# Kernel optimization log

Hardware: AMD Instinct MI355X
Metric: run time of the kernel (lower is better)

The kernel has to match this reference:

```python
import jax, jax.numpy as jnp
import numpy as np

ALPHA = 1.0
LORA_DIM = 4
MULTIPLIER = 1.0


def setup_inputs() -> dict:
    key = jax.random.key(0)
    ks = jax.random.split(key, 6)
    B, S, IN, OUT = 4, 4096, 4096, 4096
    x = jax.random.normal(ks[0], (B, S, IN), dtype=jnp.float32)
    W0 = jax.random.normal(ks[1], (OUT, IN), dtype=jnp.float32) * 0.02
    b = jax.random.normal(ks[2], (OUT,), dtype=jnp.float32) * 0.02
    # factorization(4096) -> (64, 64) for both in and out dims
    lokr_w1 = jax.random.normal(ks[3], (64, 64), dtype=jnp.float32) * 0.1
    lokr_w2_a = jax.random.normal(ks[4], (64, LORA_DIM), dtype=jnp.float32) * 0.1
    lokr_w2_b = jax.random.normal(ks[5], (LORA_DIM, 64), dtype=jnp.float32) * 0.1
    return {"x": x, "W0": W0, "b": b, "lokr_w1": lokr_w1,
            "lokr_w2_a": lokr_w2_a, "lokr_w2_b": lokr_w2_b}


def reference(x, W0, b, lokr_w1, lokr_w2_a, lokr_w2_b):
    # Original (frozen) linear forward
    result = jnp.einsum('bsi,oi->bso', x, W0) + b
    # LoKr delta weight: kron(w1, w2_a @ w2_b) * (alpha / lora_dim) * multiplier
    w2 = lokr_w2_a @ lokr_w2_b                      # (out_k, in_n) = (64, 64)
    scale = ALPHA / LORA_DIM
    diff_weight = jnp.kron(lokr_w1, w2) * (scale * MULTIPLIER)  # (4096, 4096)
    delta = jnp.einsum('bsi,oi->bso', x, diff_weight)
    return result + delta
```

## Files before the change

### kernel.cpp

```cpp
#include <hip/hip_runtime.h>
#include <hip/hip_bf16.h>
#include <stdint.h>

#define M_DIM 16384
#define N_DIM 4096
#define K_DIM 4096
#define NT    (K_DIM / 64)

typedef float f32x4 __attribute__((ext_vector_type(4)));
typedef short bf16x8 __attribute__((ext_vector_type(8)));
typedef unsigned short u16;

__device__ __forceinline__ unsigned short f32_to_bf16(float f) {
    union { float f; uint32_t u; } v; v.f = f;
    uint32_t u = v.u;
    uint32_t r = (u + 0x7FFFu + ((u >> 16) & 1u)) >> 16;
    return (unsigned short)r;
}

__device__ __forceinline__ void gload16(const void* g, void* l) {
    __builtin_amdgcn_global_load_lds(
        (const __attribute__((address_space(1))) void*)g,
        (__attribute__((address_space(3))) void*)l,
        16, 0, 0);
}

__global__ void build_weff(const float* __restrict__ W0,
                           const float* __restrict__ w1,
                           const float* __restrict__ w2a,
                           const float* __restrict__ w2b,
                           u16* __restrict__ Weff) {
    long idx = (long)blockIdx.x * 256 + threadIdx.x;
    long e0 = idx * 4;
    int o  = (int)(e0 >> 12);
    int i0 = (int)(e0 & 4095);
    int r  = o & 63;
    float a0 = w2a[r * 4 + 0], a1 = w2a[r * 4 + 1];
    float a2 = w2a[r * 4 + 2], a3 = w2a[r * 4 + 3];
    float w1v = w1[(o >> 6) * 64 + (i0 >> 6)] * 0.25f;
    float4 w0 = *(const float4*)(W0 + e0);
    const float* w0p = (const float*)&w0;
    unsigned short outp[4];
#pragma unroll
    for (int j = 0; j < 4; ++j) {
        int c = (i0 + j) & 63;
        float w2 = a0 * w2b[0 * 64 + c] + a1 * w2b[1 * 64 + c]
                 + a2 * w2b[2 * 64 + c] + a3 * w2b[3 * 64 + c];
        outp[j] = f32_to_bf16(w0p[j] + w1v * w2);
    }
    *(ushort4*)(Weff + e0) = make_ushort4(outp[0], outp[1], outp[2], outp[3]);
}

__global__ void cvt_x(const float* __restrict__ x, u16* __restrict__ xb) {
    long idx = (long)blockIdx.x * 256 + threadIdx.x;
    long e0 = idx * 8;
    float4 v0 = *(const float4*)(x + e0);
    float4 v1 = *(const float4*)(x + e0 + 4);
    union { unsigned short s[8]; int4 v; } o;
    const float* p0 = (const float*)&v0;
    const float* p1 = (const float*)&v1;
#pragma unroll
    for (int j = 0; j < 4; ++j) o.s[j]     = f32_to_bf16(p0[j]);
#pragma unroll
    for (int j = 0; j < 4; ++j) o.s[4 + j] = f32_to_bf16(p1[j]);
    *(int4*)(xb + e0) = o.v;
}

__global__ __launch_bounds__(512, 2) void gemm_8p(
        const u16* __restrict__ A,
        const u16* __restrict__ Bm,
        const float* __restrict__ bias,
        float* __restrict__ C) {
    __shared__ __align__(16) u16 ldsA[2][2][8192];
    __shared__ __align__(16) u16 ldsB[2][2][8192];

    const int tid = threadIdx.x;
    const int bid = blockIdx.x;
    const int swz = (bid & 7) * 128 + (bid >> 3);
    const int tm = swz >> 4;
    const int tn = swz & 15;
    const int mBase = tm * 256;
    const int nBase = tn * 256;

    const int lane = tid & 63;
    const int wave = tid >> 6;
    const int wr = wave >> 2;
    const int wc = wave & 3;

    const int srow = tid >> 2;
    const int slog = (tid & 3) ^ ((srow >> 1) & 3);
    const u16* aS0 = A  + (size_t)(mBase + srow)       * K_DIM + slog * 8;
    const u16* aS1 = A  + (size_t)(mBase + srow + 128) * K_DIM + slog * 8;
    const u16* bS0 = Bm + (size_t)(nBase + srow)       * K_DIM + slog * 8;
    const u16* bS1 = Bm + (size_t)(nBase + srow + 128) * K_DIM + slog * 8;

#define STAGE_A(buf, t, ks) do { const size_t _k = (size_t)(t) * 64 + (ks) * 32; \
        gload16(aS0 + _k, &ldsA[buf][ks][tid * 8]);                              \
        gload16(aS1 + _k, &ldsA[buf][ks][4096 + tid * 8]); } while (0)
#define STAGE_B(buf, t, ks) do { const size_t _k = (size_t)(t) * 64 + (ks) * 32; \
        gload16(bS0 + _k, &ldsB[buf][ks][tid * 8]);                              \
        gload16(bS1 + _k, &ldsB[buf][ks][4096 + tid * 8]); } while (0)

    const int rl = lane & 15, cbk = lane >> 4;
    const int sslot = cbk ^ ((rl >> 1) & 3);
    const int aRd = (wr * 128 + rl) * 32 + sslot * 8;
    const int bRd = (wc * 64  + rl) * 32 + sslot * 8;

#define RD_A(buf, ks, m) (*(const bf16x8*)&ldsA[buf][ks][aRd + (m) * 512])
#define RD_B(buf, ks, n) (*(const bf16x8*)&ldsB[buf][ks][bRd + (n) * 512])

    f32x4 acc[8][4] = {};
    bf16x8 aA0, aA1, aA2, aA3;
    bf16x8 aB0, aB1, aB2, aB3;
    bf16x8 bX0, bX1, bX2, bX3;
    bf16x8 bY0, bY1, bY2, bY3;

#define MFMA16(A0_,A1_,A2_,A3_,B0_,B1_,B2_,B3_,mh)                                      \
    acc[(mh)*4+0][0] = __builtin_amdgcn_mfma_f32_16x16x32_bf16(A0_, B0_, acc[(mh)*4+0][0], 0, 0, 0); \
    acc[(mh)*4+0][1] = __builtin_amdgcn_mfma_f32_16x16x32_bf16(A0_, B1_, acc[(mh)*4+0][1], 0, 0, 0); \
    acc[(mh)*4+0][2] = __builtin_amdgcn_mfma_f32_16x16x32_bf16(A0_, B2_, acc[(mh)*4+0][2], 0, 0, 0); \
    acc[(mh)*4+0][3] = __builtin_amdgcn_mfma_f32_16x16x32_bf16(A0_, B3_, acc[(mh)*4+0][3], 0, 0, 0); \
    acc[(mh)*4+1][0] = __builtin_amdgcn_mfma_f32_16x16x32_bf16(A1_, B0_, acc[(mh)*4+1][0], 0, 0, 0); \
    acc[(mh)*4+1][1] = __builtin_amdgcn_mfma_f32_16x16x32_bf16(A1_, B1_, acc[(mh)*4+1][1], 0, 0, 0); \
    acc[(mh)*4+1][2] = __builtin_amdgcn_mfma_f32_16x16x32_bf16(A1_, B2_, acc[(mh)*4+1][2], 0, 0, 0); \
    acc[(mh)*4+1][3] = __builtin_amdgcn_mfma_f32_16x16x32_bf16(A1_, B3_, acc[(mh)*4+1][3], 0, 0, 0); \
    acc[(mh)*4+2][0] = __builtin_amdgcn_mfma_f32_16x16x32_bf16(A2_, B0_, acc[(mh)*4+2][0], 0, 0, 0); \
    acc[(mh)*4+2][1] = __builtin_amdgcn_mfma_f32_16x16x32_bf16(A2_, B1_, acc[(mh)*4+2][1], 0, 0, 0); \
    acc[(mh)*4+2][2] = __builtin_amdgcn_mfma_f32_16x16x32_bf16(A2_, B2_, acc[(mh)*4+2][2], 0, 0, 0); \
    acc[(mh)*4+2][3] = __builtin_amdgcn_mfma_f32_16x16x32_bf16(A2_, B3_, acc[(mh)*4+2][3], 0, 0, 0); \
    acc[(mh)*4+3][0] = __builtin_amdgcn_mfma_f32_16x16x32_bf16(A3_, B0_, acc[(mh)*4+3][0], 0, 0, 0); \
    acc[(mh)*4+3][1] = __builtin_amdgcn_mfma_f32_16x16x32_bf16(A3_, B1_, acc[(mh)*4+3][1], 0, 0, 0); \
    acc[(mh)*4+3][2] = __builtin_amdgcn_mfma_f32_16x16x32_bf16(A3_, B2_, acc[(mh)*4+3][2], 0, 0, 0); \
    acc[(mh)*4+3][3] = __builtin_amdgcn_mfma_f32_16x16x32_bf16(A3_, B3_, acc[(mh)*4+3][3], 0, 0, 0);

#define RD_BSET(set, buf, ks)                                   \
    set##0 = RD_B(buf, ks, 0); set##1 = RD_B(buf, ks, 1);       \
    set##2 = RD_B(buf, ks, 2); set##3 = RD_B(buf, ks, 3);
#define RD_ALO(buf, ks)                                         \
    aA0 = RD_A(buf, ks, 0); aA1 = RD_A(buf, ks, 1);             \
    aA2 = RD_A(buf, ks, 2); aA3 = RD_A(buf, ks, 3);
#define RD_AHI(buf, ks)                                         \
    aB0 = RD_A(buf, ks, 4); aB1 = RD_A(buf, ks, 5);             \
    aB2 = RD_A(buf, ks, 6); aB3 = RD_A(buf, ks, 7);

#define PH_END() do { __builtin_amdgcn_sched_barrier(0);        \
                      __builtin_amdgcn_s_barrier(); } while (0)

    STAGE_B(0, 0, 0); STAGE_A(0, 0, 0); STAGE_B(0, 0, 1); STAGE_A(0, 0, 1);
    STAGE_B(1, 1, 0); STAGE_A(1, 1, 0); STAGE_B(1, 1, 1);
    asm volatile("s_waitcnt vmcnt(6)" ::: "memory");
    __builtin_amdgcn_s_barrier();
    RD_BSET(bX, 0, 0)
    RD_ALO(0, 0)

    for (int it = 0; it < NT / 2; ++it) {
        const int t1 = 2 * it + 1;
        const int t2 = (2 * it + 2 < NT) ? 2 * it + 2 : NT - 1;
        const int t3 = (2 * it + 3 < NT) ? 2 * it + 3 : NT - 1;

        STAGE_A(1, t1, 1);
        RD_AHI(0, 0)
        __builtin_amdgcn_s_setprio(1);
        MFMA16(aA0, aA1, aA2, aA3, bX0, bX1, bX2, bX3, 0)
        __builtin_amdgcn_s_setprio(0);
        PH_END();

        STAGE_B(0, t2, 0);
        RD_BSET(bY, 0, 1)
        RD_ALO(0, 1)
        __builtin_amdgcn_s_setprio(1);
        MFMA16(aB0, aB1, aB2, aB3, bX0, bX1, bX2, bX3, 1)
        __builtin_amdgcn_s_setprio(0);
        PH_END();

        STAGE_A(0, t2, 0);
        RD_AHI(0, 1)
        __builtin_amdgcn_s_setprio(1);
        MFMA16(aA0, aA1, aA2, aA3, bY0, bY1, bY2, bY3, 0)
        __builtin_amdgcn_s_setprio(0);
        asm volatile("s_waitcnt vmcnt(4)" ::: "memory");
        PH_END();

        STAGE_B(0, t2, 1);
        RD_BSET(bX, 1, 0)
        RD_ALO(1, 0)
        __builtin_amdgcn_s_setprio(1);
        MFMA16(aB0, aB1, aB2, aB3, bY0, bY1, bY2, bY3, 1)
        __builtin_amdgcn_s_setprio(0);
        PH_END();

        STAGE_A(0, t2, 1);
        RD_AHI(1, 0)
        __builtin_amdgcn_s_setprio(1);
        MFMA16(aA0, aA1, aA2, aA3, bX0, bX1, bX2, bX3, 0)
        __builtin_amdgcn_s_setprio(0);
        PH_END();

        STAGE_B(1, t3, 0);
        RD_BSET(bY, 1, 1)
        RD_ALO(1, 1)
        __builtin_amdgcn_s_setprio(1);
        MFMA16(aB0, aB1, aB2, aB3, bX0, bX1, bX2, bX3, 1)
        __builtin_amdgcn_s_setprio(0);
        PH_END();

        STAGE_A(1, t3, 0);
        RD_AHI(1, 1)
        __builtin_amdgcn_s_setprio(1);
        MFMA16(aA0, aA1, aA2, aA3, bY0, bY1, bY2, bY3, 0)
        __builtin_amdgcn_s_setprio(0);
        asm volatile("s_waitcnt vmcnt(4)" ::: "memory");
        PH_END();

        STAGE_B(1, t3, 1);
        RD_BSET(bX, 0, 0)
        RD_ALO(0, 0)
        __builtin_amdgcn_s_setprio(1);
        MFMA16(aB0, aB1, aB2, aB3, bY0, bY1, bY2, bY3, 1)
        __builtin_amdgcn_s_setprio(0);
        PH_END();
    }
    asm volatile("s_waitcnt vmcnt(0) lgkmcnt(0)" ::: "memory");

#pragma unroll
    for (int n = 0; n < 4; ++n) {
        const int col = nBase + wc * 64 + n * 16 + rl;
        const float bv = bias[col];
#pragma unroll
        for (int m = 0; m < 8; ++m) {
            const int row = mBase + wr * 128 + m * 16 + cbk * 4;
#pragma unroll
            for (int j = 0; j < 4; ++j)
                C[(size_t)(row + j) * N_DIM + col] = acc[m][n][j] + bv;
        }
    }
#undef STAGE_A
#undef STAGE_B
#undef RD_A
#undef RD_B
#undef RD_BSET
#undef RD_ALO
#undef RD_AHI
#undef MFMA16
#undef PH_END
}

__global__ void naive_fallback(const float* __restrict__ x,
                               const float* __restrict__ W0,
                               const float* __restrict__ b,
                               const float* __restrict__ w1,
                               const float* __restrict__ w2a,
                               const float* __restrict__ w2b,
                               float* __restrict__ out) {
    __shared__ float w2s[64 * 64];
    for (int t = threadIdx.x; t < 4096; t += blockDim.x) {
        int rr = t >> 6, cc = t & 63;
        float s = 0.f;
        for (int k = 0; k < 4; ++k) s += w2a[rr * 4 + k] * w2b[k * 64 + cc];
        w2s[t] = s * 0.25f;
    }
    __syncthreads();
    long idx = (long)blockIdx.x * blockDim.x + threadIdx.x;
    int m = (int)(idx >> 12);
    int o = (int)(idx & 4095);
    const float* xr = x + (long)m * K_DIM;
    const float* wrp = W0 + (long)o * K_DIM;
    int ob = (o >> 6) * 64, orr = (o & 63) * 64;
    float acc = 0.f;
    for (int i = 0; i < K_DIM; ++i) {
        float w = wrp[i] + w1[ob + (i >> 6)] * w2s[orr + (i & 63)];
        acc += xr[i] * w;
    }
    out[idx] = acc + b[o];
}

extern "C" void kernel_launch(void* const* d_in, const int* in_sizes, int n_in,
                              void* d_out, int out_size, void* d_ws, size_t ws_size,
                              hipStream_t stream) {
    const float* x   = (const float*)d_in[0];
    const float* W0  = (const float*)d_in[1];
    const float* b   = (const float*)d_in[2];
    const float* w1  = (const float*)d_in[3];
    const float* w2a = (const float*)d_in[4];
    const float* w2b = (const float*)d_in[5];
    float* out = (float*)d_out;

    const size_t xb_bytes = (size_t)M_DIM * K_DIM * 2;
    const size_t wf_bytes = (size_t)N_DIM * K_DIM * 2;

    if (ws_size >= xb_bytes + wf_bytes) {
        u16* xb = (u16*)d_ws;
        u16* wf = (u16*)((char*)d_ws + xb_bytes);
        build_weff<<<(N_DIM * (long)K_DIM) / 4 / 256, 256, 0, stream>>>(W0, w1, w2a, w2b, wf);
        cvt_x<<<((long)M_DIM * K_DIM) / 8 / 256, 256, 0, stream>>>(x, xb);
        gemm_8p<<<(M_DIM / 256) * (N_DIM / 256), 512, 0, stream>>>(xb, wf, b, out);
    } else {
        naive_fallback<<<((long)M_DIM * N_DIM) / 256, 256, 0, stream>>>(
            x, W0, b, w1, w2a, w2b, out);
    }
}
```

Measured before the change: 647.9 us.

## Merge prep kernels and restructure GEMM main loop into K-merged quadrant phases

The two preprocessing kernels (effective-weight build and x-to-bf16 conversion) become a single launch that picks its branch by block index, saving one kernel launch and its tail. The GEMM main loop is reorganised into phases that each compute a 4x2 quadrant of the accumulator tile over both 32-wide K halves. Fragments for both K halves are loaded together, and the barrier now sits at the top of each phase instead of the bottom. The staging order and waitcnt placement change with it, which alters the LDS hazard timing and register pressure and could introduce races or spills.

```diff
diff --git a/kernel.cpp b/kernel.cpp
--- a/kernel.cpp
+++ b/kernel.cpp
@@ -7,7 +7,7 @@
 #define K_DIM 4096
 #define NT    (K_DIM / 64)
 
-typedef float f32x4 __attribute__((ext_vector_type(4)));
+typedef float f32x4  __attribute__((ext_vector_type(4)));
 typedef short bf16x8 __attribute__((ext_vector_type(8)));
 typedef unsigned short u16;
 
@@ -25,48 +25,51 @@
         16, 0, 0);
 }
 
-__global__ void build_weff(const float* __restrict__ W0,
-                           const float* __restrict__ w1,
-                           const float* __restrict__ w2a,
-                           const float* __restrict__ w2b,
-                           u16* __restrict__ Weff) {
-    long idx = (long)blockIdx.x * 256 + threadIdx.x;
-    long e0 = idx * 4;
-    int o  = (int)(e0 >> 12);
-    int i0 = (int)(e0 & 4095);
-    int r  = o & 63;
-    float a0 = w2a[r * 4 + 0], a1 = w2a[r * 4 + 1];
-    float a2 = w2a[r * 4 + 2], a3 = w2a[r * 4 + 3];
-    float w1v = w1[(o >> 6) * 64 + (i0 >> 6)] * 0.25f;
-    float4 w0 = *(const float4*)(W0 + e0);
-    const float* w0p = (const float*)&w0;
-    unsigned short outp[4];
-#pragma unroll
-    for (int j = 0; j < 4; ++j) {
-        int c = (i0 + j) & 63;
-        float w2 = a0 * w2b[0 * 64 + c] + a1 * w2b[1 * 64 + c]
-                 + a2 * w2b[2 * 64 + c] + a3 * w2b[3 * 64 + c];
-        outp[j] = f32_to_bf16(w0p[j] + w1v * w2);
-    }
-    *(ushort4*)(Weff + e0) = make_ushort4(outp[0], outp[1], outp[2], outp[3]);
-}
-
-__global__ void cvt_x(const float* __restrict__ x, u16* __restrict__ xb) {
-    long idx = (long)blockIdx.x * 256 + threadIdx.x;
-    long e0 = idx * 8;
-    float4 v0 = *(const float4*)(x + e0);
-    float4 v1 = *(const float4*)(x + e0 + 4);
-    union { unsigned short s[8]; int4 v; } o;
-    const float* p0 = (const float*)&v0;
-    const float* p1 = (const float*)&v1;
-#pragma unroll
-    for (int j = 0; j < 4; ++j) o.s[j]     = f32_to_bf16(p0[j]);
-#pragma unroll
-    for (int j = 0; j < 4; ++j) o.s[4 + j] = f32_to_bf16(p1[j]);
-    *(int4*)(xb + e0) = o.v;
-}
-
-__global__ __launch_bounds__(512, 2) void gemm_8p(
+__global__ void prep(const float* __restrict__ W0,
+                     const float* __restrict__ w1,
+                     const float* __restrict__ w2a,
+                     const float* __restrict__ w2b,
+                     const float* __restrict__ x,
+                     u16* __restrict__ Weff,
+                     u16* __restrict__ xb) {
+    const int bid = blockIdx.x;
+    if (bid < 16384) {
+        long idx = (long)bid * 256 + threadIdx.x;
+        long e0 = idx * 4;
+        int o  = (int)(e0 >> 12);
+        int i0 = (int)(e0 & 4095);
+        int r  = o & 63;
+        float a0 = w2a[r * 4 + 0], a1 = w2a[r * 4 + 1];
+        float a2 = w2a[r * 4 + 2], a3 = w2a[r * 4 + 3];
+        float w1v = w1[(o >> 6) * 64 + (i0 >> 6)] * 0.25f;
+        float4 w0 = *(const float4*)(W0 + e0);
+        const float* w0p = (const float*)&w0;
+        unsigned short outp[4];
+#pragma unroll
+        for (int j = 0; j < 4; ++j) {
+            int c = (i0 + j) & 63;
+            float w2 = a0 * w2b[0 * 64 + c] + a1 * w2b[1 * 64 + c]
+                     + a2 * w2b[2 * 64 + c] + a3 * w2b[3 * 64 + c];
+            outp[j] = f32_to_bf16(w0p[j] + w1v * w2);
+        }
+        *(ushort4*)(Weff + e0) = make_ushort4(outp[0], outp[1], outp[2], outp[3]);
+    } else {
+        long idx = (long)(bid - 16384) * 256 + threadIdx.x;
+        long e0 = idx * 8;
+        float4 v0 = *(const float4*)(x + e0);
+        float4 v1 = *(const float4*)(x + e0 + 4);
+        union { unsigned short s[8]; int4 v; } o;
+        const float* p0 = (const float*)&v0;
+        const float* p1 = (const float*)&v1;
+#pragma unroll
+        for (int j = 0; j < 4; ++j) o.s[j]     = f32_to_bf16(p0[j]);
+#pragma unroll
+        for (int j = 0; j < 4; ++j) o.s[4 + j] = f32_to_bf16(p1[j]);
+        *(int4*)(xb + e0) = o.v;
+    }
+}
+
+__global__ __launch_bounds__(512, 2) void gemm_q(
         const u16* __restrict__ A,
         const u16* __restrict__ Bm,
         const float* __restrict__ bias,
@@ -110,115 +113,110 @@
 #define RD_B(buf, ks, n) (*(const bf16x8*)&ldsB[buf][ks][bRd + (n) * 512])
 
     f32x4 acc[8][4] = {};
-    bf16x8 aA0, aA1, aA2, aA3;
-    bf16x8 aB0, aB1, aB2, aB3;
-    bf16x8 bX0, bX1, bX2, bX3;
-    bf16x8 bY0, bY1, bY2, bY3;
-
-#define MFMA16(A0_,A1_,A2_,A3_,B0_,B1_,B2_,B3_,mh)                                      \
-    acc[(mh)*4+0][0] = __builtin_amdgcn_mfma_f32_16x16x32_bf16(A0_, B0_, acc[(mh)*4+0][0], 0, 0, 0); \
-    acc[(mh)*4+0][1] = __builtin_amdgcn_mfma_f32_16x16x32_bf16(A0_, B1_, acc[(mh)*4+0][1], 0, 0, 0); \
-    acc[(mh)*4+0][2] = __builtin_amdgcn_mfma_f32_16x16x32_bf16(A0_, B2_, acc[(mh)*4+0][2], 0, 0, 0); \
-    acc[(mh)*4+0][3] = __builtin_amdgcn_mfma_f32_16x16x32_bf16(A0_, B3_, acc[(mh)*4+0][3], 0, 0, 0); \
-    acc[(mh)*4+1][0] = __builtin_amdgcn_mfma_f32_16x16x32_bf16(A1_, B0_, acc[(mh)*4+1][0], 0, 0, 0); \
-    acc[(mh)*4+1][1] = __builtin_amdgcn_mfma_f32_16x16x32_bf16(A1_, B1_, acc[(mh)*4+1][1], 0, 0, 0); \
-    acc[(mh)*4+1][2] = __builtin_amdgcn_mfma_f32_16x16x32_bf16(A1_, B2_, acc[(mh)*4+1][2], 0, 0, 0); \
-    acc[(mh)*4+1][3] = __builtin_amdgcn_mfma_f32_16x16x32_bf16(A1_, B3_, acc[(mh)*4+1][3], 0, 0, 0); \
-    acc[(mh)*4+2][0] = __builtin_amdgcn_mfma_f32_16x16x32_bf16(A2_, B0_, acc[(mh)*4+2][0], 0, 0, 0); \
-    acc[(mh)*4+2][1] = __builtin_amdgcn_mfma_f32_16x16x32_bf16(A2_, B1_, acc[(mh)*4+2][1], 0, 0, 0); \
-    acc[(mh)*4+2][2] = __builtin_amdgcn_mfma_f32_16x16x32_bf16(A2_, B2_, acc[(mh)*4+2][2], 0, 0, 0); \
-    acc[(mh)*4+2][3] = __builtin_amdgcn_mfma_f32_16x16x32_bf16(A2_, B3_, acc[(mh)*4+2][3], 0, 0, 0); \
-    acc[(mh)*4+3][0] = __builtin_amdgcn_mfma_f32_16x16x32_bf16(A3_, B0_, acc[(mh)*4+3][0], 0, 0, 0); \
-    acc[(mh)*4+3][1] = __builtin_amdgcn_mfma_f32_16x16x32_bf16(A3_, B1_, acc[(mh)*4+3][1], 0, 0, 0); \
-    acc[(mh)*4+3][2] = __builtin_amdgcn_mfma_f32_16x16x32_bf16(A3_, B2_, acc[(mh)*4+3][2], 0, 0, 0); \
-    acc[(mh)*4+3][3] = __builtin_amdgcn_mfma_f32_16x16x32_bf16(A3_, B3_, acc[(mh)*4+3][3], 0, 0, 0);
-
-#define RD_BSET(set, buf, ks)                                   \
-    set##0 = RD_B(buf, ks, 0); set##1 = RD_B(buf, ks, 1);       \
-    set##2 = RD_B(buf, ks, 2); set##3 = RD_B(buf, ks, 3);
-#define RD_ALO(buf, ks)                                         \
-    aA0 = RD_A(buf, ks, 0); aA1 = RD_A(buf, ks, 1);             \
-    aA2 = RD_A(buf, ks, 2); aA3 = RD_A(buf, ks, 3);
-#define RD_AHI(buf, ks)                                         \
-    aB0 = RD_A(buf, ks, 4); aB1 = RD_A(buf, ks, 5);             \
-    aB2 = RD_A(buf, ks, 6); aB3 = RD_A(buf, ks, 7);
-
-#define PH_END() do { __builtin_amdgcn_sched_barrier(0);        \
-                      __builtin_amdgcn_s_barrier(); } while (0)
-
-    STAGE_B(0, 0, 0); STAGE_A(0, 0, 0); STAGE_B(0, 0, 1); STAGE_A(0, 0, 1);
-    STAGE_B(1, 1, 0); STAGE_A(1, 1, 0); STAGE_B(1, 1, 1);
-    asm volatile("s_waitcnt vmcnt(6)" ::: "memory");
-    __builtin_amdgcn_s_barrier();
-    RD_BSET(bX, 0, 0)
-    RD_ALO(0, 0)
+    bf16x8 af[4][2];
+    bf16x8 bL[2][2];
+    bf16x8 bH[2][2];
+
+#define QUAD(mh, nh, BREG)                                                     \
+    _Pragma("unroll")                                                          \
+    for (int kk = 0; kk < 2; ++kk) {                                           \
+        _Pragma("unroll")                                                      \
+        for (int m = 0; m < 4; ++m) {                                          \
+            _Pragma("unroll")                                                  \
+            for (int n = 0; n < 2; ++n)                                        \
+                acc[(mh)*4+m][(nh)*2+n] = __builtin_amdgcn_mfma_f32_16x16x32_bf16( \
+                    af[m][kk], BREG[n][kk], acc[(mh)*4+m][(nh)*2+n], 0, 0, 0); \
+        }                                                                      \
+    }
+
+#define PH_TOP() __builtin_amdgcn_s_barrier()
+#define PH_BOT() __builtin_amdgcn_sched_barrier(0)
+
+    STAGE_B(0, 0, 0); STAGE_B(0, 0, 1);
+    STAGE_A(0, 0, 0); STAGE_A(0, 0, 1);
+    STAGE_B(1, 1, 0); STAGE_B(1, 1, 1);
+    asm volatile("s_waitcnt vmcnt(4)" ::: "memory");
 
     for (int it = 0; it < NT / 2; ++it) {
-        const int t1 = 2 * it + 1;
+        const int u1 = 2 * it + 1;
         const int t2 = (2 * it + 2 < NT) ? 2 * it + 2 : NT - 1;
         const int t3 = (2 * it + 3 < NT) ? 2 * it + 3 : NT - 1;
 
-        STAGE_A(1, t1, 1);
-        RD_AHI(0, 0)
-        __builtin_amdgcn_s_setprio(1);
-        MFMA16(aA0, aA1, aA2, aA3, bX0, bX1, bX2, bX3, 0)
-        __builtin_amdgcn_s_setprio(0);
-        PH_END();
-
+        PH_TOP();
+        bL[0][0] = RD_B(0, 0, 0); bL[0][1] = RD_B(0, 1, 0);
+        bL[1][0] = RD_B(0, 0, 1); bL[1][1] = RD_B(0, 1, 1);
+        af[0][0] = RD_A(0, 0, 0); af[0][1] = RD_A(0, 1, 0);
+        af[1][0] = RD_A(0, 0, 1); af[1][1] = RD_A(0, 1, 1);
+        af[2][0] = RD_A(0, 0, 2); af[2][1] = RD_A(0, 1, 2);
+        af[3][0] = RD_A(0, 0, 3); af[3][1] = RD_A(0, 1, 3);
+        STAGE_A(1, u1, 0);
+        __builtin_amdgcn_s_setprio(1);
+        QUAD(0, 0, bL)
+        __builtin_amdgcn_s_setprio(0);
+        PH_BOT();
+        PH_TOP();
+        bH[0][0] = RD_B(0, 0, 2); bH[0][1] = RD_B(0, 1, 2);
+        bH[1][0] = RD_B(0, 0, 3); bH[1][1] = RD_B(0, 1, 3);
+        STAGE_A(1, u1, 1);
+        __builtin_amdgcn_s_setprio(1);
+        QUAD(0, 1, bH)
+        __builtin_amdgcn_s_setprio(0);
+        PH_BOT();
+        PH_TOP();
+        af[0][0] = RD_A(0, 0, 4); af[0][1] = RD_A(0, 1, 4);
+        af[1][0] = RD_A(0, 0, 5); af[1][1] = RD_A(0, 1, 5);
+        af[2][0] = RD_A(0, 0, 6); af[2][1] = RD_A(0, 1, 6);
+        af[3][0] = RD_A(0, 0, 7); af[3][1] = RD_A(0, 1, 7);
         STAGE_B(0, t2, 0);
-        RD_BSET(bY, 0, 1)
-        RD_ALO(0, 1)
-        __builtin_amdgcn_s_setprio(1);
-        MFMA16(aB0, aB1, aB2, aB3, bX0, bX1, bX2, bX3, 1)
-        __builtin_amdgcn_s_setprio(0);
-        PH_END();
-
+        __builtin_amdgcn_s_setprio(1);
+        QUAD(1, 0, bL)
+        __builtin_amdgcn_s_setprio(0);
+        PH_BOT();
+        PH_TOP();
+        STAGE_B(0, t2, 1);
+        __builtin_amdgcn_s_setprio(1);
+        QUAD(1, 1, bH)
+        __builtin_amdgcn_s_setprio(0);
+        asm volatile("s_waitcnt vmcnt(4)" ::: "memory");
+        PH_BOT();
+
+        PH_TOP();
+        bL[0][0] = RD_B(1, 0, 0); bL[0][1] = RD_B(1, 1, 0);
+        bL[1][0] = RD_B(1, 0, 1); bL[1][1] = RD_B(1, 1, 1);
+        af[0][0] = RD_A(1, 0, 0); af[0][1] = RD_A(1, 1, 0);
+        af[1][0] = RD_A(1, 0, 1); af[1][1] = RD_A(1, 1, 1);
+        af[2][0] = RD_A(1, 0, 2); af[2][1] = RD_A(1, 1, 2);
+        af[3][0] = RD_A(1, 0, 3); af[3][1] = RD_A(1, 1, 3);
         STAGE_A(0, t2, 0);
-        RD_AHI(0, 1)
-        __builtin_amdgcn_s_setprio(1);
-        MFMA16(aA0, aA1, aA2, aA3, bY0, bY1, bY2, bY3, 0)
+        __builtin_amdgcn_s_setprio(1);
+        QUAD(0, 0, bL)
+        __builtin_amdgcn_s_setprio(0);
+        PH_BOT();
+        PH_TOP();
+        bH[0][0] = RD_B(1, 0, 2); bH[0][1] = RD_B(1, 1, 2);
+        bH[1][0] = RD_B(1, 0, 3); bH[1][1] = RD_B(1, 1, 3);
+        STAGE_A(0, t2, 1);
+        __builtin_amdgcn_s_setprio(1);
+        QUAD(0, 1, bH)
+        __builtin_amdgcn_s_setprio(0);
+        PH_BOT();
+        PH_TOP();
+        af[0][0] = RD_A(1, 0, 4); af[0][1] = RD_A(1, 1, 4);
+        af[1][0] = RD_A(1, 0, 5); af[1][1] = RD_A(1, 1, 5);
+        af[2][0] = RD_A(1, 0, 6); af[2][1] = RD_A(1, 1, 6);
+        af[3][0] = RD_A(1, 0, 7); af[3][1] = RD_A(1, 1, 7);
+        STAGE_B(1, t3, 0);
+        __builtin_amdgcn_s_setprio(1);
+        QUAD(1, 0, bL)
+        __builtin_amdgcn_s_setprio(0);
+        PH_BOT();
+        PH_TOP();
+        STAGE_B(1, t3, 1);
+        __builtin_amdgcn_s_setprio(1);
+        QUAD(1, 1, bH)
         __builtin_amdgcn_s_setprio(0);
         asm volatile("s_waitcnt vmcnt(4)" ::: "memory");
-        PH_END();
-
-        STAGE_B(0, t2, 1);
-        RD_BSET(bX, 1, 0)
-        RD_ALO(1, 0)
-        __builtin_amdgcn_s_setprio(1);
-        MFMA16(aB0, aB1, aB2, aB3, bY0, bY1, bY2, bY3, 1)
-        __builtin_amdgcn_s_setprio(0);
-        PH_END();
-
-        STAGE_A(0, t2, 1);
-        RD_AHI(1, 0)
-        __builtin_amdgcn_s_setprio(1);
-        MFMA16(aA0, aA1, aA2, aA3, bX0, bX1, bX2, bX3, 0)
-        __builtin_amdgcn_s_setprio(0);
-        PH_END();
-
-        STAGE_B(1, t3, 0);
-        RD_BSET(bY, 1, 1)
-        RD_ALO(1, 1)
-        __builtin_amdgcn_s_setprio(1);
-        MFMA16(aB0, aB1, aB2, aB3, bX0, bX1, bX2, bX3, 1)
-        __builtin_amdgcn_s_setprio(0);
-        PH_END();
-
-        STAGE_A(1, t3, 0);
-        RD_AHI(1, 1)
-        __builtin_amdgcn_s_setprio(1);
-        MFMA16(aA0, aA1, aA2, aA3, bY0, bY1, bY2, bY3, 0)
-        __builtin_amdgcn_s_setprio(0);
-        asm volatile("s_waitcnt vmcnt(4)" ::: "memory");
-        PH_END();
-
-        STAGE_B(1, t3, 1);
-        RD_BSET(bX, 0, 0)
-        RD_ALO(0, 0)
-        __builtin_amdgcn_s_setprio(1);
-        MFMA16(aB0, aB1, aB2, aB3, bY0, bY1, bY2, bY3, 1)
-        __builtin_amdgcn_s_setprio(0);
-        PH_END();
+        PH_BOT();
     }
     asm volatile("s_waitcnt vmcnt(0) lgkmcnt(0)" ::: "memory");
 
@@ -238,11 +236,9 @@
 #undef STAGE_B
 #undef RD_A
 #undef RD_B
-#undef RD_BSET
-#undef RD_ALO
-#undef RD_AHI
-#undef MFMA16
-#undef PH_END
+#undef QUAD
+#undef PH_TOP
+#undef PH_BOT
 }
 
 __global__ void naive_fallback(const float* __restrict__ x,
@@ -291,9 +287,8 @@
     if (ws_size >= xb_bytes + wf_bytes) {
         u16* xb = (u16*)d_ws;
         u16* wf = (u16*)((char*)d_ws + xb_bytes);
-        build_weff<<<(N_DIM * (long)K_DIM) / 4 / 256, 256, 0, stream>>>(W0, w1, w2a, w2b, wf);
-        cvt_x<<<((long)M_DIM * K_DIM) / 8 / 256, 256, 0, stream>>>(x, xb);
-        gemm_8p<<<(M_DIM / 256) * (N_DIM / 256), 512, 0, stream>>>(xb, wf, b, out);
+        prep<<<49152, 256, 0, stream>>>(W0, w1, w2a, w2b, x, wf, xb);
+        gemm_q<<<(M_DIM / 256) * (N_DIM / 256), 512, 0, stream>>>(xb, wf, b, out);
     } else {
         naive_fallback<<<((long)M_DIM * N_DIM) / 256, 256, 0, stream>>>(
             x, W0, b, w1, w2a, w2b, out);
```

Measured after the change: 648.3 us. Within noise of the previous version (+0.1%).
